# Kernel tuning notes

Hardware: AMD Instinct MI355X
Metric: run time of the kernel (lower is better)

Reference implementation:

```python
import jax, jax.numpy as jnp
import numpy as np

H = 4          # num attention heads
C1 = 64        # channel_num[0]
C2 = 128       # channel_num[1]
KV = C1 + C2   # 192
MLP = C1 * 4   # expand_ratio=4


def _layernorm(x, g, b, eps=1e-6):
    m = jnp.mean(x, axis=-1, keepdims=True)
    v = jnp.mean((x - m) ** 2, axis=-1, keepdims=True)
    return (x - m) * jax.lax.rsqrt(v + eps) * g + b


def setup_inputs() -> dict:
    key = jax.random.key(0)
    ks = jax.random.split(key, 12)
    B, N = 8, 3136
    s_q = 1.0 / np.sqrt(C1)
    s_kv = 1.0 / np.sqrt(KV)
    return {
        "emb1": jax.random.normal(ks[0], (B, N, C1), jnp.float32),
        "emb2": jax.random.normal(ks[1], (B, N, C2), jnp.float32),
        # per-head projection weights (nn.Linear convention: y = x @ W.T)
        "Wq": jax.random.uniform(ks[2], (H, C1, C1), jnp.float32, -s_q, s_q),
        "Wk": jax.random.uniform(ks[3], (H, KV, KV), jnp.float32, -s_kv, s_kv),
        "Wv": jax.random.uniform(ks[4], (H, KV, KV), jnp.float32, -s_kv, s_kv),
        "Wout": jax.random.uniform(ks[5], (C1, C1), jnp.float32, -s_q, s_q),
        "ln1_g": jnp.ones((C1,), jnp.float32),
        "ln1_b": jnp.zeros((C1,), jnp.float32),
        "lnall_g": jnp.ones((KV,), jnp.float32),
        "lnall_b": jnp.zeros((KV,), jnp.float32),
        "ffn_g": jnp.ones((C1,), jnp.float32),
        "ffn_b": jnp.zeros((C1,), jnp.float32),
        "fc1_w": jax.random.uniform(ks[6], (MLP, C1), jnp.float32, -s_q, s_q),
        "fc1_b": jnp.zeros((MLP,), jnp.float32),
        "fc2_w": jax.random.uniform(ks[7], (C1, MLP), jnp.float32, -1.0 / np.sqrt(MLP), 1.0 / np.sqrt(MLP)),
        "fc2_b": jnp.zeros((C1,), jnp.float32),
    }


def reference(emb1, emb2, Wq, Wk, Wv, Wout, ln1_g, ln1_b, lnall_g, lnall_b,
              ffn_g, ffn_b, fc1_w, fc1_b, fc2_w, fc2_b):
    # emb1: [B,N,C1], emb2: [B,N,C2]
    emb_all = jnp.concatenate([emb1, emb2], axis=2)          # [B,N,KV]
    cx1 = _layernorm(emb1, ln1_g, ln1_b)                     # [B,N,C1]
    ea = _layernorm(emb_all, lnall_g, lnall_b)               # [B,N,KV]

    # batched per-head projections (replaces Python loop over ModuleList)
    qT = jnp.einsum('bnc,hdc->bhdn', cx1, Wq)                # [B,H,C1,N]
    k = jnp.einsum('bnk,hdk->bhnd', ea, Wk)                  # [B,H,N,KV]
    vT = jnp.einsum('bnk,hdk->bhdn', ea, Wv)                 # [B,H,KV,N]

    scores = jnp.einsum('bhcn,bhnk->bhck', qT, k) / np.sqrt(KV)  # [B,H,C1,KV]
    # InstanceNorm2d over spatial dims (C1, KV) per (batch, head), affine=False
    m = jnp.mean(scores, axis=(2, 3), keepdims=True)
    v = jnp.mean((scores - m) ** 2, axis=(2, 3), keepdims=True)
    scores = (scores - m) * jax.lax.rsqrt(v + 1e-5)
    probs = jax.nn.softmax(scores, axis=3)                   # softmax over KV

    ctx = jnp.einsum('bhck,bhkn->bhcn', probs, vT)           # [B,H,C1,N]
    ctx = jnp.mean(ctx, axis=1).transpose(0, 2, 1)           # mean over heads -> [B,N,C1]
    o = ctx @ Wout.T                                         # [B,N,C1]

    cx = emb1 + o                                            # residual
    x = _layernorm(cx, ffn_g, ffn_b)
    x = jax.nn.gelu(x @ fc1_w.T + fc1_b, approximate=False)
    x = x @ fc2_w.T + fc2_b
    return x + cx
```

## Files before the change

### kernel.cpp

```cpp
#include <hip/hip_runtime.h>
#include <hip/hip_bf16.h>

typedef __hip_bfloat16 bf;
typedef unsigned short ushort_t;
typedef __attribute__((ext_vector_type(8))) short short8;
typedef __attribute__((ext_vector_type(4))) float f32x4;

#define NB 8
#define SEQ 3136
#define HD 4

__device__ __forceinline__ float lo_bf(unsigned u){ return __uint_as_float(u << 16); }
__device__ __forceinline__ float hi_bf(unsigned u){ return __uint_as_float(u & 0xffff0000u); }
__device__ __forceinline__ float b16f(ushort_t s){ return __uint_as_float(((unsigned)s) << 16); }
__device__ __forceinline__ unsigned short f2bfbits(float f){
  unsigned u = __float_as_uint(f);
  unsigned r = u + 0x7fffu + ((u >> 16) & 1u);
  return (unsigned short)(r >> 16);
}
__device__ __forceinline__ float ldin(const void* p, long i, bool isbf){
  return isbf ? __bfloat162float(((const bf*)p)[i]) : ((const float*)p)[i];
}
__device__ __forceinline__ float4 ld4(const void* p, long i, bool isbf){
  if (isbf){
    uint2 u = *reinterpret_cast<const uint2*>((const unsigned short*)p + i);
    return make_float4(lo_bf(u.x), hi_bf(u.x), lo_bf(u.y), hi_bf(u.y));
  }
  const float* f = (const float*)p + i;
  return make_float4(f[0], f[1], f[2], f[3]);
}
__device__ __forceinline__ short8 ldfrag(const void* p, long i, bool isbf){
  if (isbf) return *reinterpret_cast<const short8*>((const unsigned short*)p + i);
  const float* f = (const float*)p + i;
  short8 r;
  #pragma unroll
  for (int q=0;q<8;++q) r[q] = (short)f2bfbits(f[q]);
  return r;
}
#define DTYPE_FLAG(p) (((const unsigned*)(p))[0] == 0x3F803F80u)

__device__ __forceinline__ float wsum(float v){
  #pragma unroll
  for (int o = 32; o > 0; o >>= 1) v += __shfl_xor(v, o, 64);
  return v;
}
__device__ __forceinline__ float wmax(float v){
  #pragma unroll
  for (int o = 32; o > 0; o >>= 1) v = fmaxf(v, __shfl_xor(v, o, 64));
  return v;
}

__global__ __launch_bounds__(256) void k_g(
    const void* __restrict__ emb1, const void* __restrict__ emb2,
    const void* __restrict__ g1, const void* __restrict__ b1,
    const void* __restrict__ ga, const void* __restrict__ ba,
    ushort_t* __restrict__ part, ushort_t* __restrict__ eag){
  bool isbf = DTYPE_FLAG(g1);
  __shared__ __align__(16) ushort_t z1t[64*72];
  __shared__ __align__(16) ushort_t zat[192*72];
  int tid = threadIdx.x, wave = tid >> 6, lane = tid & 63;
  int quad = lane >> 4, nl = lane & 15;
  int b = blockIdx.y, ch = blockIdx.x;
  long t0 = (long)b*SEQ + ch*64;
  float g1l = ldin(g1,lane,isbf), b1l = ldin(b1,lane,isbf);
  float ga0 = ldin(ga,lane,isbf),     ba0 = ldin(ba,lane,isbf);
  float ga1 = ldin(ga,64+lane,isbf),  ba1 = ldin(ba,64+lane,isbf);
  float ga2 = ldin(ga,128+lane,isbf), ba2 = ldin(ba,128+lane,isbf);
  #pragma unroll 4
  for (int k = 0; k < 16; ++k){
    int tok = wave*16 + k;
    long t = t0 + tok;
    float e1  = ldin(emb1, t*64 + lane, isbf);
    float e2a = ldin(emb2, t*128 + lane, isbf);
    float e2b = ldin(emb2, t*128 + 64 + lane, isbf);
    float s1 = wsum(e1), ss1 = wsum(e1*e1);
    float m1 = s1*(1.f/64.f);
    float r1 = rsqrtf(fmaxf(ss1*(1.f/64.f) - m1*m1, 0.f) + 1e-6f);
    z1t[lane*72 + tok] = f2bfbits((e1 - m1)*r1*g1l + b1l);
    float s23 = wsum(e2a+e2b), ss23 = wsum(e2a*e2a + e2b*e2b);
    float ma = (s1+s23)*(1.f/192.f);
    float ra = rsqrtf(fmaxf((ss1+ss23)*(1.f/192.f) - ma*ma, 0.f) + 1e-6f);
    unsigned short za0 = f2bfbits((e1  - ma)*ra*ga0 + ba0);
    unsigned short za1 = f2bfbits((e2a - ma)*ra*ga1 + ba1);
    unsigned short za2 = f2bfbits((e2b - ma)*ra*ga2 + ba2);
    zat[lane*72 + tok]       = za0;
    zat[(64+lane)*72 + tok]  = za1;
    zat[(128+lane)*72 + tok] = za2;
    eag[t*192 + lane]       = za0;
    eag[t*192 + 64 + lane]  = za1;
    eag[t*192 + 128 + lane] = za2;
  }
  __syncthreads();
  short8 a0 = *reinterpret_cast<const short8*>(&z1t[(wave*16+nl)*72 + quad*8]);
  short8 a1 = *reinterpret_cast<const short8*>(&z1t[(wave*16+nl)*72 + 32 + quad*8]);
  ushort_t* P = part + ((long)b*49 + ch)*12288;
  #pragma unroll
  for (int nt = 0; nt < 12; ++nt){
    f32x4 cd = {0.f,0.f,0.f,0.f};
    short8 b0 = *reinterpret_cast<const short8*>(&zat[(nt*16+nl)*72 + quad*8]);
    cd = __builtin_amdgcn_mfma_f32_16x16x32_bf16(a0, b0, cd, 0, 0, 0);
    short8 b1v = *reinterpret_cast<const short8*>(&zat[(nt*16+nl)*72 + 32 + quad*8]);
    cd = __builtin_amdgcn_mfma_f32_16x16x32_bf16(a1, b1v, cd, 0, 0, 0);
    #pragma unroll
    for (int reg = 0; reg < 4; ++reg)
      P[(wave*16 + quad*4 + reg)*192 + nt*16 + nl] = f2bfbits(cd[reg]);
  }
}

__global__ __launch_bounds__(64) void k_red(
    const ushort_t* __restrict__ part, float* __restrict__ G){
  int idx4 = blockIdx.x*64 + threadIdx.x;
  int b = idx4 / 3072, e4 = idx4 - b*3072;
  const ushort_t* p = part + (long)b*49*12288 + e4*4;
  float s0=0.f, s1=0.f, s2=0.f, s3=0.f;
  #pragma unroll
  for (int ch = 0; ch < 49; ++ch){
    uint2 u = *reinterpret_cast<const uint2*>(p + (long)ch*12288);
    s0 += lo_bf(u.x); s1 += hi_bf(u.x); s2 += lo_bf(u.y); s3 += hi_bf(u.y);
  }
  ((float4*)G)[idx4] = make_float4(s0,s1,s2,s3);
}

__global__ __launch_bounds__(256) void k_s(
    const float* __restrict__ G, const void* __restrict__ Wq, const void* __restrict__ Wk,
    const void* __restrict__ lng, float* __restrict__ S){
  bool isbf = DTYPE_FLAG(lng);
  __shared__ __align__(16) ushort_t sGb[64*200];
  __shared__ __align__(16) ushort_t sT[48*72];
  int ec = blockIdx.x, h = blockIdx.y, b = blockIdx.z;
  int e0 = ec*48;
  int tid = threadIdx.x, wave = tid >> 6, lane = tid & 63;
  int quad = lane >> 4, nl = lane & 15;
  const float4* Gb4 = (const float4*)(G + (long)b*12288);
  for (int i16 = tid; i16 < 3072; i16 += 256){
    float4 v = Gb4[i16];
    int e = i16*4; int c = e/192, j = e - c*192;
    unsigned lo = (unsigned)f2bfbits(v.x) | ((unsigned)f2bfbits(v.y) << 16);
    unsigned hi = (unsigned)f2bfbits(v.z) | ((unsigned)f2bfbits(v.w) << 16);
    *reinterpret_cast<uint2*>(&sGb[c*200 + j]) = make_uint2(lo, hi);
  }
  __syncthreads();
  long wk0 = (long)h*36864;
  short8 aG[6];
  #pragma unroll
  for (int ks = 0; ks < 6; ++ks)
    aG[ks] = *reinterpret_cast<const short8*>(&sGb[(wave*16+nl)*200 + ks*32 + quad*8]);
  #pragma unroll
  for (int nt = 0; nt < 3; ++nt){
    f32x4 cd = {0.f,0.f,0.f,0.f};
    #pragma unroll
    for (int ks = 0; ks < 6; ++ks){
      short8 bw = ldfrag(Wk, wk0 + (long)(e0 + nt*16+nl)*192 + ks*32 + quad*8, isbf);
      cd = __builtin_amdgcn_mfma_f32_16x16x32_bf16(aG[ks], bw, cd, 0, 0, 0);
    }
    #pragma unroll
    for (int reg = 0; reg < 4; ++reg)
      sT[(nt*16+nl)*72 + wave*16 + quad*4 + reg] = f2bfbits(cd[reg]);
  }
  __syncthreads();
  long wq0 = (long)h*4096;
  short8 aQ[2];
  #pragma unroll
  for (int ks = 0; ks < 2; ++ks)
    aQ[ks] = ldfrag(Wq, wq0 + (long)(wave*16+nl)*64 + ks*32 + quad*8, isbf);
  const float scale = 0.07216878364870323f;
  float* Sb = S + ((long)b*HD + h)*12288;
  #pragma unroll
  for (int nt = 0; nt < 3; ++nt){
    f32x4 cd = {0.f,0.f,0.f,0.f};
    #pragma unroll
    for (int ks = 0; ks < 2; ++ks){
      short8 bt = *reinterpret_cast<const short8*>(&sT[(nt*16+nl)*72 + ks*32 + quad*8]);
      cd = __builtin_amdgcn_mfma_f32_16x16x32_bf16(aQ[ks], bt, cd, 0, 0, 0);
    }
    #pragma unroll
    for (int reg = 0; reg < 4; ++reg)
      Sb[(wave*16 + quad*4 + reg)*192 + e0 + nt*16 + nl] = cd[reg]*scale;
  }
}

__global__ __launch_bounds__(256) void k_smpv(
    const float* __restrict__ S, const void* __restrict__ Wv,
    const void* __restrict__ lng, float* __restrict__ Mh){
  bool isbf = DTYPE_FLAG(lng);
  __shared__ __align__(16) float sP[64*196];
  __shared__ __align__(16) unsigned sWv[192*52];
  __shared__ float red[8];
  __shared__ float stat[2];
  int jc = blockIdx.x, h = blockIdx.y, b = blockIdx.z;
  const float* Sb = S + ((long)b*HD + h)*12288;
  int tid = threadIdx.x, wave = tid >> 6, lane = tid & 63;
  long wv0 = (long)h*36864;
  float ps = 0.f, pss = 0.f;
  const float4* Sb4 = (const float4*)Sb;
  for (int i16 = tid; i16 < 3072; i16 += 256){
    float4 v = Sb4[i16];
    int e = i16*4; int c = e/192, j = e - c*192;
    *reinterpret_cast<float4*>(&sP[c*196 + j]) = v;
    ps += v.x + v.y + v.z + v.w;
    pss += v.x*v.x + v.y*v.y + v.z*v.z + v.w*v.w;
  }
  if (isbf){
    const unsigned short* wvp = (const unsigned short*)Wv + wv0 + jc*96;
    for (int idx = tid; idx < 4608; idx += 256){
      int r = idx/24, c2 = idx - r*24;
      uint2 v = *reinterpret_cast<const uint2*>(wvp + (long)r*192 + c2*4);
      *reinterpret_cast<uint2*>(&sWv[r*52 + c2*2]) = v;
    }
  } else {
    for (int idx = tid; idx < 9216; idx += 256){
      int r = idx/48, c = idx - r*48;
      float a0 = ldin(Wv, wv0 + (long)r*192 + jc*96 + c*2,     false);
      float a1 = ldin(Wv, wv0 + (long)r*192 + jc*96 + c*2 + 1, false);
      sWv[r*52 + c] = (unsigned)f2bfbits(a0) | ((unsigned)f2bfbits(a1) << 16);
    }
  }
  ps = wsum(ps); pss = wsum(pss);
  if (lane == 0){ red[wave] = ps; red[4+wave] = pss; }
  __syncthreads();
  if (tid == 0){
    float s  = red[0]+red[1]+red[2]+red[3];
    float s2 = red[4]+red[5]+red[6]+red[7];
    float m = s * (1.f/12288.f);
    stat[0] = m;
    stat[1] = rsqrtf(fmaxf(s2*(1.f/12288.f) - m*m, 0.f) + 1e-5f);
  }
  __syncthreads();
  float m = stat[0], r = stat[1];
  for (int rr = 0; rr < 16; ++rr){
    int row = wave*16 + rr;
    float v0 = (sP[row*196+lane]     - m)*r;
    float v1 = (sP[row*196+64+lane]  - m)*r;
    float v2 = (sP[row*196+128+lane] - m)*r;
    float mx = wmax(fmaxf(v0, fmaxf(v1, v2)));
    float e0 = __expf(v0-mx), e1 = __expf(v1-mx), e2 = __expf(v2-mx);
    float inv = 1.f / wsum(e0+e1+e2);
    sP[row*196+lane]     = e0*inv;
    sP[row*196+64+lane]  = e1*inv;
    sP[row*196+128+lane] = e2*inv;
  }
  __syncthreads();
  int ty = tid >> 4, tx = tid & 15;
  int j0 = jc*96 + tx*6;
  float acc[4][6];
  #pragma unroll
  for (int i=0;i<4;++i) for (int q=0;q<6;++q) acc[i][q]=0.f;
  #pragma unroll 2
  for (int e = 0; e < 192; ++e){
    float p4[4];
    #pragma unroll
    for (int i=0;i<4;++i) p4[i] = sP[(ty*4+i)*196 + e];
    unsigned wa = sWv[e*52 + tx*3];
    unsigned wb = sWv[e*52 + tx*3 + 1];
    unsigned wc = sWv[e*52 + tx*3 + 2];
    float w0 = lo_bf(wa), w1 = hi_bf(wa), w2 = lo_bf(wb),
          w3 = hi_bf(wb), w4 = lo_bf(wc), w5 = hi_bf(wc);
    #pragma unroll
    for (int i=0;i<4;++i){
      acc[i][0] = fmaf(p4[i], w0, acc[i][0]);
      acc[i][1] = fmaf(p4[i], w1, acc[i][1]);
      acc[i][2] = fmaf(p4[i], w2, acc[i][2]);
      acc[i][3] = fmaf(p4[i], w3, acc[i][3]);
      acc[i][4] = fmaf(p4[i], w4, acc[i][4]);
      acc[i][5] = fmaf(p4[i], w5, acc[i][5]);
    }
  }
  float* Mb = Mh + ((long)b*HD + h)*12288;
  #pragma unroll
  for (int i=0;i<4;++i)
    #pragma unroll
    for (int q=0;q<6;++q)
      Mb[(ty*4+i)*192 + j0 + q] = acc[i][q];
}

__global__ __launch_bounds__(256) void k_w2(
    const float* __restrict__ Mh, const void* __restrict__ Wout,
    const void* __restrict__ lng, ushort_t* __restrict__ W2){
  bool isbf = DTYPE_FLAG(lng);
  __shared__ __align__(16) float sM[64*49];
  int jc = blockIdx.x, b = blockIdx.y;
  int tid = threadIdx.x;
  for (int idx = tid; idx < 3072; idx += 256){
    int c = idx/48, j = idx - c*48;
    long base = (long)b*HD*12288 + c*192 + jc*48 + j;
    float s = Mh[base] + Mh[base+12288] + Mh[base+2*12288] + Mh[base+3*12288];
    sM[c*49 + j] = 0.25f*s;
  }
  __syncthreads();
  int ty = tid >> 4, tx = tid & 15;
  float acc[4][3];
  #pragma unroll
  for (int i=0;i<4;++i) for (int q=0;q<3;++q) acc[i][q]=0.f;
  for (int c = 0; c < 64; c += 4){
    float4 w4[4];
    #pragma unroll
    for (int i=0;i<4;++i) w4[i] = ld4(Wout, (long)(ty*4+i)*64 + c, isbf);
    float ww[4][4];
    #pragma unroll
    for (int i=0;i<4;++i){ ww[i][0]=w4[i].x; ww[i][1]=w4[i].y; ww[i][2]=w4[i].z; ww[i][3]=w4[i].w; }
    #pragma unroll
    for (int u = 0; u < 4; ++u){
      float t3[3];
      #pragma unroll
      for (int q=0;q<3;++q) t3[q] = sM[(c+u)*49 + tx*3 + q];
      #pragma unroll
      for (int i=0;i<4;++i)
        #pragma unroll
        for (int q=0;q<3;++q) acc[i][q] = fmaf(ww[i][u], t3[q], acc[i][q]);
    }
  }
  ushort_t* W2b = W2 + (long)b*12288;
  #pragma unroll
  for (int i=0;i<4;++i)
    #pragma unroll
    for (int q=0;q<3;++q)
      W2b[(ty*4+i)*192 + jc*48 + tx*3 + q] = f2bfbits(acc[i][q]);
}

__global__ __launch_bounds__(256) void k_tail(
    const void* __restrict__ emb1, const ushort_t* __restrict__ eag,
    const ushort_t* __restrict__ W2g,
    const void* __restrict__ ffg, const void* __restrict__ ffb,
    const void* __restrict__ f1w, const void* __restrict__ f1b,
    const void* __restrict__ f2w, const void* __restrict__ f2b,
    const void* __restrict__ lng, void* __restrict__ out){
  bool isbf = DTYPE_FLAG(lng);
  __shared__ __align__(16) ushort_t sCX[16*72];
  __shared__ __align__(16) ushort_t sX[16*88];
  __shared__ __align__(16) ushort_t sH[16*280];
  int tid = threadIdx.x, wave = tid >> 6, lane = tid & 63;
  int quad = lane >> 4, nl = lane & 15;
  int b = blockIdx.y;
  long tbase = (long)b*SEQ + blockIdx.x*16;

  short8 aO[6];
  #pragma unroll
  for (int kt = 0; kt < 6; ++kt)
    aO[kt] = *reinterpret_cast<const short8*>(eag + (tbase + nl)*192 + kt*32 + quad*8);
  const ushort_t* W2b = W2g + (long)b*12288;
  {
    f32x4 cd = {0.f,0.f,0.f,0.f};
    #pragma unroll
    for (int kt = 0; kt < 6; ++kt){
      short8 bf8 = *reinterpret_cast<const short8*>(W2b + (wave*16+nl)*192 + kt*32 + quad*8);
      cd = __builtin_amdgcn_mfma_f32_16x16x32_bf16(aO[kt], bf8, cd, 0, 0, 0);
    }
    #pragma unroll
    for (int reg = 0; reg < 4; ++reg){
      int tokl = quad*4 + reg;
      int chn = wave*16 + nl;
      float e1v = ldin(emb1, (tbase + tokl)*64 + chn, isbf);
      sCX[tokl*72 + chn] = f2bfbits(cd[reg] + e1v);
    }
  }
  __syncthreads();

  float gl = ldin(ffg, lane, isbf), bl = ldin(ffb, lane, isbf);
  #pragma unroll
  for (int k = 0; k < 4; ++k){
    int tokl = wave*4 + k;
    float c = b16f(sCX[tokl*72 + lane]);
    float s = wsum(c), ss = wsum(c*c);
    float m = s*(1.f/64.f);
    float r = rsqrtf(fmaxf(ss*(1.f/64.f) - m*m, 0.f) + 1e-6f);
    sX[tokl*88 + lane] = f2bfbits((c - m)*r*gl + bl);
  }
  __syncthreads();

  short8 aX[2];
  #pragma unroll
  for (int kt = 0; kt < 2; ++kt)
    aX[kt] = *reinterpret_cast<const short8*>(&sX[nl*88 + kt*32 + quad*8]);
  #pragma unroll
  for (int nn = 0; nn < 4; ++nn){
    int nt = wave*4 + nn;
    f32x4 cd = {0.f,0.f,0.f,0.f};
    #pragma unroll
    for (int kt = 0; kt < 2; ++kt){
      short8 bf8 = ldfrag(f1w, (long)(nt*16+nl)*64 + kt*32 + quad*8, isbf);
      cd = __builtin_amdgcn_mfma_f32_16x16x32_bf16(aX[kt], bf8, cd, 0, 0, 0);
    }
    float bb = ldin(f1b, nt*16+nl, isbf);
    #pragma unroll
    for (int reg = 0; reg < 4; ++reg){
      float v = cd[reg] + bb;
      float h = 0.5f*v*(1.f + erff(v*0.70710678118654752f));
      sH[(quad*4 + reg)*280 + nt*16 + nl] = f2bfbits(h);
    }
  }
  __syncthreads();

  short8 aH[8];
  #pragma unroll
  for (int kt = 0; kt < 8; ++kt)
    aH[kt] = *reinterpret_cast<const short8*>(&sH[nl*280 + kt*32 + quad*8]);
  {
    f32x4 cd = {0.f,0.f,0.f,0.f};
    #pragma unroll
    for (int kt = 0; kt < 8; ++kt){
      short8 bf8 = ldfrag(f2w, (long)(wave*16+nl)*256 + kt*32 + quad*8, isbf);
      cd = __builtin_amdgcn_mfma_f32_16x16x32_bf16(aH[kt], bf8, cd, 0, 0, 0);
    }
    float bb2 = ldin(f2b, wave*16+nl, isbf);
    #pragma unroll
    for (int reg = 0; reg < 4; ++reg){
      int tokl = quad*4 + reg;
      int chn = wave*16 + nl;
      float y = cd[reg] + bb2 + b16f(sCX[tokl*72 + chn]);
      if (isbf) sCX[tokl*72 + chn] = f2bfbits(y);
      else ((float*)out)[(tbase + tokl)*64 + chn] = y;
    }
  }
  if (isbf){
    __syncthreads();
    int tokl = wave*4 + (lane >> 4), prt = lane & 15;
    uint2 v = *reinterpret_cast<const uint2*>(&sCX[tokl*72 + prt*4]);
    *reinterpret_cast<uint2*>((ushort_t*)out + (tbase + tokl)*64 + prt*4) = v;
  }
}

extern "C" void kernel_launch(void* const* d_in, const int* in_sizes, int n_in,
                              void* d_out, int out_size, void* d_ws, size_t ws_size,
                              hipStream_t stream){
  const void* emb1 = d_in[0];
  const void* emb2 = d_in[1];
  const void* Wq   = d_in[2];
  const void* Wk   = d_in[3];
  const void* Wv   = d_in[4];
  const void* Wout = d_in[5];
  const void* ln1g = d_in[6];
  const void* ln1b = d_in[7];
  const void* lag  = d_in[8];
  const void* lab  = d_in[9];
  const void* ffg  = d_in[10];
  const void* ffb  = d_in[11];
  const void* f1w  = d_in[12];
  const void* f1b  = d_in[13];
  const void* f2w  = d_in[14];
  const void* f2b  = d_in[15];

  char* base = (char*)d_ws;
  ushort_t* part = (ushort_t*)base;
  ushort_t* ea   = (ushort_t*)(base + 9633792);
  float*    G    = (float*)(base + 19267584);
  float*    S    = (float*)(base + 19660800);
  float*    Mh   = (float*)(base + 21233664);
  ushort_t* W2   = (ushort_t*)(base + 22806528);

  k_g   <<<dim3(49,NB),   256, 0, stream>>>(emb1, emb2, ln1g, ln1b, lag, lab, part, ea);
  k_red <<<384,            64, 0, stream>>>(part, G);
  k_s   <<<dim3(4,HD,NB), 256, 0, stream>>>(G, Wq, Wk, ln1g, S);
  k_smpv<<<dim3(2,HD,NB), 256, 0, stream>>>(S, Wv, ln1g, Mh);
  k_w2  <<<dim3(4,NB),    256, 0, stream>>>(Mh, Wout, ln1g, W2);
  k_tail<<<dim3(196,NB),  256, 0, stream>>>(emb1, ea, W2, ffg, ffb,
                                            f1w, f1b, f2w, f2b, ln1g, d_out);
}
```

Measured before the change: 206.2 us.

## Fuse score, softmax and PV into one attention kernel; pre-convert weights to bf16

Merges k_s and k_smpv into a single k_att kernel per (head,batch), so scores stay in shared memory instead of a global round-trip. The PV product moves from scalar FMA to MFMA, with probabilities split into hi/lo bf16 halves to keep precision. Extra blocks in k_g convert the weights once to bf16 (Wv transposed) so later kernels load bf16 fragments directly. The cost is that k_att launches only 32 blocks, so there is less parallelism in that stage.

```diff
diff --git a/kernel.cpp b/kernel.cpp
--- a/kernel.cpp
+++ b/kernel.cpp
@@ -29,13 +29,8 @@
   const float* f = (const float*)p + i;
   return make_float4(f[0], f[1], f[2], f[3]);
 }
-__device__ __forceinline__ short8 ldfrag(const void* p, long i, bool isbf){
-  if (isbf) return *reinterpret_cast<const short8*>((const unsigned short*)p + i);
-  const float* f = (const float*)p + i;
-  short8 r;
-  #pragma unroll
-  for (int q=0;q<8;++q) r[q] = (short)f2bfbits(f[q]);
-  return r;
+__device__ __forceinline__ ushort_t cvt1(const void* p, long i, bool isbf){
+  return isbf ? ((const ushort_t*)p)[i] : f2bfbits(((const float*)p)[i]);
 }
 #define DTYPE_FLAG(p) (((const unsigned*)(p))[0] == 0x3F803F80u)
 
@@ -54,13 +49,33 @@
     const void* __restrict__ emb1, const void* __restrict__ emb2,
     const void* __restrict__ g1, const void* __restrict__ b1,
     const void* __restrict__ ga, const void* __restrict__ ba,
-    ushort_t* __restrict__ part, ushort_t* __restrict__ eag){
+    const void* __restrict__ Wq, const void* __restrict__ Wk, const void* __restrict__ Wv,
+    const void* __restrict__ f1w, const void* __restrict__ f2w,
+    ushort_t* __restrict__ part, ushort_t* __restrict__ eag,
+    ushort_t* __restrict__ Wqb, ushort_t* __restrict__ Wkb, ushort_t* __restrict__ WvTb,
+    ushort_t* __restrict__ f1wb, ushort_t* __restrict__ f2wb){
   bool isbf = DTYPE_FLAG(g1);
+  int tid = threadIdx.x;
+  int b = blockIdx.y, ch = blockIdx.x;
+  if (ch >= 49){
+    if (b != 0) return;
+    int g = (ch - 49)*256 + tid;
+    const int STR = 24*256;
+    for (int i = g; i < 16384; i += STR) Wqb[i] = cvt1(Wq, i, isbf);
+    for (int i = g; i < 147456; i += STR) Wkb[i] = cvt1(Wk, i, isbf);
+    for (int i = g; i < 147456; i += STR){
+      int hh = i / 36864, r = i - hh*36864;
+      int j = r / 192, e = r - j*192;
+      WvTb[i] = cvt1(Wv, (long)hh*36864 + e*192 + j, isbf);
+    }
+    for (int i = g; i < 16384; i += STR) f1wb[i] = cvt1(f1w, i, isbf);
+    for (int i = g; i < 16384; i += STR) f2wb[i] = cvt1(f2w, i, isbf);
+    return;
+  }
   __shared__ __align__(16) ushort_t z1t[64*72];
   __shared__ __align__(16) ushort_t zat[192*72];
-  int tid = threadIdx.x, wave = tid >> 6, lane = tid & 63;
+  int wave = tid >> 6, lane = tid & 63;
   int quad = lane >> 4, nl = lane & 15;
-  int b = blockIdx.y, ch = blockIdx.x;
   long t0 = (long)b*SEQ + ch*64;
   float g1l = ldin(g1,lane,isbf), b1l = ldin(b1,lane,isbf);
   float ga0 = ldin(ga,lane,isbf),     ba0 = ldin(ba,lane,isbf);
@@ -108,7 +123,7 @@
 }
 
 __global__ __launch_bounds__(64) void k_red(
-    const ushort_t* __restrict__ part, float* __restrict__ G){
+    const ushort_t* __restrict__ part, ushort_t* __restrict__ Gb){
   int idx4 = blockIdx.x*64 + threadIdx.x;
   int b = idx4 / 3072, e4 = idx4 - b*3072;
   const ushort_t* p = part + (long)b*49*12288 + e4*4;
@@ -118,39 +133,37 @@
     uint2 u = *reinterpret_cast<const uint2*>(p + (long)ch*12288);
     s0 += lo_bf(u.x); s1 += hi_bf(u.x); s2 += lo_bf(u.y); s3 += hi_bf(u.y);
   }
-  ((float4*)G)[idx4] = make_float4(s0,s1,s2,s3);
-}
-
-__global__ __launch_bounds__(256) void k_s(
-    const float* __restrict__ G, const void* __restrict__ Wq, const void* __restrict__ Wk,
-    const void* __restrict__ lng, float* __restrict__ S){
-  bool isbf = DTYPE_FLAG(lng);
-  __shared__ __align__(16) ushort_t sGb[64*200];
-  __shared__ __align__(16) ushort_t sT[48*72];
-  int ec = blockIdx.x, h = blockIdx.y, b = blockIdx.z;
-  int e0 = ec*48;
+  unsigned lo = (unsigned)f2bfbits(s0) | ((unsigned)f2bfbits(s1) << 16);
+  unsigned hi = (unsigned)f2bfbits(s2) | ((unsigned)f2bfbits(s3) << 16);
+  *reinterpret_cast<uint2*>(Gb + (long)idx4*4) = make_uint2(lo, hi);
+}
+
+__global__ __launch_bounds__(256) void k_att(
+    const ushort_t* __restrict__ Gb, const ushort_t* __restrict__ Wqb,
+    const ushort_t* __restrict__ Wkb, const ushort_t* __restrict__ WvTb,
+    float* __restrict__ Mh){
+  __shared__ __align__(16) ushort_t sT[192*72];
+  __shared__ __align__(16) float    sS[64*196];
+  __shared__ __align__(16) ushort_t sPh[64*200];
+  __shared__ __align__(16) ushort_t sPl[64*200];
+  __shared__ float red[8];
+  __shared__ float stat[2];
+  int h = blockIdx.x, b = blockIdx.y;
   int tid = threadIdx.x, wave = tid >> 6, lane = tid & 63;
   int quad = lane >> 4, nl = lane & 15;
-  const float4* Gb4 = (const float4*)(G + (long)b*12288);
-  for (int i16 = tid; i16 < 3072; i16 += 256){
-    float4 v = Gb4[i16];
-    int e = i16*4; int c = e/192, j = e - c*192;
-    unsigned lo = (unsigned)f2bfbits(v.x) | ((unsigned)f2bfbits(v.y) << 16);
-    unsigned hi = (unsigned)f2bfbits(v.z) | ((unsigned)f2bfbits(v.w) << 16);
-    *reinterpret_cast<uint2*>(&sGb[c*200 + j]) = make_uint2(lo, hi);
-  }
-  __syncthreads();
-  long wk0 = (long)h*36864;
+
+  const ushort_t* Gp = Gb + (long)b*12288;
   short8 aG[6];
   #pragma unroll
   for (int ks = 0; ks < 6; ++ks)
-    aG[ks] = *reinterpret_cast<const short8*>(&sGb[(wave*16+nl)*200 + ks*32 + quad*8]);
-  #pragma unroll
-  for (int nt = 0; nt < 3; ++nt){
+    aG[ks] = *reinterpret_cast<const short8*>(Gp + (wave*16+nl)*192 + ks*32 + quad*8);
+  const ushort_t* Wkp = Wkb + (long)h*36864;
+  #pragma unroll
+  for (int nt = 0; nt < 12; ++nt){
     f32x4 cd = {0.f,0.f,0.f,0.f};
     #pragma unroll
     for (int ks = 0; ks < 6; ++ks){
-      short8 bw = ldfrag(Wk, wk0 + (long)(e0 + nt*16+nl)*192 + ks*32 + quad*8, isbf);
+      short8 bw = *reinterpret_cast<const short8*>(Wkp + (nt*16+nl)*192 + ks*32 + quad*8);
       cd = __builtin_amdgcn_mfma_f32_16x16x32_bf16(aG[ks], bw, cd, 0, 0, 0);
     }
     #pragma unroll
@@ -158,15 +171,16 @@
       sT[(nt*16+nl)*72 + wave*16 + quad*4 + reg] = f2bfbits(cd[reg]);
   }
   __syncthreads();
-  long wq0 = (long)h*4096;
+
+  const ushort_t* Wqp = Wqb + (long)h*4096;
   short8 aQ[2];
   #pragma unroll
   for (int ks = 0; ks < 2; ++ks)
-    aQ[ks] = ldfrag(Wq, wq0 + (long)(wave*16+nl)*64 + ks*32 + quad*8, isbf);
+    aQ[ks] = *reinterpret_cast<const short8*>(Wqp + (wave*16+nl)*64 + ks*32 + quad*8);
   const float scale = 0.07216878364870323f;
-  float* Sb = S + ((long)b*HD + h)*12288;
-  #pragma unroll
-  for (int nt = 0; nt < 3; ++nt){
+  float ps = 0.f, pss = 0.f;
+  #pragma unroll
+  for (int nt = 0; nt < 12; ++nt){
     f32x4 cd = {0.f,0.f,0.f,0.f};
     #pragma unroll
     for (int ks = 0; ks < 2; ++ks){
@@ -174,45 +188,10 @@
       cd = __builtin_amdgcn_mfma_f32_16x16x32_bf16(aQ[ks], bt, cd, 0, 0, 0);
     }
     #pragma unroll
-    for (int reg = 0; reg < 4; ++reg)
-      Sb[(wave*16 + quad*4 + reg)*192 + e0 + nt*16 + nl] = cd[reg]*scale;
-  }
-}
-
-__global__ __launch_bounds__(256) void k_smpv(
-    const float* __restrict__ S, const void* __restrict__ Wv,
-    const void* __restrict__ lng, float* __restrict__ Mh){
-  bool isbf = DTYPE_FLAG(lng);
-  __shared__ __align__(16) float sP[64*196];
-  __shared__ __align__(16) unsigned sWv[192*52];
-  __shared__ float red[8];
-  __shared__ float stat[2];
-  int jc = blockIdx.x, h = blockIdx.y, b = blockIdx.z;
-  const float* Sb = S + ((long)b*HD + h)*12288;
-  int tid = threadIdx.x, wave = tid >> 6, lane = tid & 63;
-  long wv0 = (long)h*36864;
-  float ps = 0.f, pss = 0.f;
-  const float4* Sb4 = (const float4*)Sb;
-  for (int i16 = tid; i16 < 3072; i16 += 256){
-    float4 v = Sb4[i16];
-    int e = i16*4; int c = e/192, j = e - c*192;
-    *reinterpret_cast<float4*>(&sP[c*196 + j]) = v;
-    ps += v.x + v.y + v.z + v.w;
-    pss += v.x*v.x + v.y*v.y + v.z*v.z + v.w*v.w;
-  }
-  if (isbf){
-    const unsigned short* wvp = (const unsigned short*)Wv + wv0 + jc*96;
-    for (int idx = tid; idx < 4608; idx += 256){
-      int r = idx/24, c2 = idx - r*24;
-      uint2 v = *reinterpret_cast<const uint2*>(wvp + (long)r*192 + c2*4);
-      *reinterpret_cast<uint2*>(&sWv[r*52 + c2*2]) = v;
-    }
-  } else {
-    for (int idx = tid; idx < 9216; idx += 256){
-      int r = idx/48, c = idx - r*48;
-      float a0 = ldin(Wv, wv0 + (long)r*192 + jc*96 + c*2,     false);
-      float a1 = ldin(Wv, wv0 + (long)r*192 + jc*96 + c*2 + 1, false);
-      sWv[r*52 + c] = (unsigned)f2bfbits(a0) | ((unsigned)f2bfbits(a1) << 16);
+    for (int reg = 0; reg < 4; ++reg){
+      float v = cd[reg]*scale;
+      sS[(wave*16 + quad*4 + reg)*196 + nt*16 + nl] = v;
+      ps += v; pss += v*v;
     }
   }
   ps = wsum(ps); pss = wsum(pss);
@@ -227,50 +206,44 @@
   }
   __syncthreads();
   float m = stat[0], r = stat[1];
+  #pragma unroll 2
   for (int rr = 0; rr < 16; ++rr){
     int row = wave*16 + rr;
-    float v0 = (sP[row*196+lane]     - m)*r;
-    float v1 = (sP[row*196+64+lane]  - m)*r;
-    float v2 = (sP[row*196+128+lane] - m)*r;
+    float v0 = (sS[row*196+lane]     - m)*r;
+    float v1 = (sS[row*196+64+lane]  - m)*r;
+    float v2 = (sS[row*196+128+lane] - m)*r;
     float mx = wmax(fmaxf(v0, fmaxf(v1, v2)));
     float e0 = __expf(v0-mx), e1 = __expf(v1-mx), e2 = __expf(v2-mx);
     float inv = 1.f / wsum(e0+e1+e2);
-    sP[row*196+lane]     = e0*inv;
-    sP[row*196+64+lane]  = e1*inv;
-    sP[row*196+128+lane] = e2*inv;
-  }
-  __syncthreads();
-  int ty = tid >> 4, tx = tid & 15;
-  int j0 = jc*96 + tx*6;
-  float acc[4][6];
-  #pragma unroll
-  for (int i=0;i<4;++i) for (int q=0;q<6;++q) acc[i][q]=0.f;
-  #pragma unroll 2
-  for (int e = 0; e < 192; ++e){
-    float p4[4];
-    #pragma unroll
-    for (int i=0;i<4;++i) p4[i] = sP[(ty*4+i)*196 + e];
-    unsigned wa = sWv[e*52 + tx*3];
-    unsigned wb = sWv[e*52 + tx*3 + 1];
-    unsigned wc = sWv[e*52 + tx*3 + 2];
-    float w0 = lo_bf(wa), w1 = hi_bf(wa), w2 = lo_bf(wb),
-          w3 = hi_bf(wb), w4 = lo_bf(wc), w5 = hi_bf(wc);
-    #pragma unroll
-    for (int i=0;i<4;++i){
-      acc[i][0] = fmaf(p4[i], w0, acc[i][0]);
-      acc[i][1] = fmaf(p4[i], w1, acc[i][1]);
-      acc[i][2] = fmaf(p4[i], w2, acc[i][2]);
-      acc[i][3] = fmaf(p4[i], w3, acc[i][3]);
-      acc[i][4] = fmaf(p4[i], w4, acc[i][4]);
-      acc[i][5] = fmaf(p4[i], w5, acc[i][5]);
-    }
-  }
+    e0 *= inv; e1 *= inv; e2 *= inv;
+    ushort_t h0 = f2bfbits(e0), h1 = f2bfbits(e1), h2 = f2bfbits(e2);
+    sPh[row*200+lane]     = h0;  sPl[row*200+lane]     = f2bfbits(e0 - b16f(h0));
+    sPh[row*200+64+lane]  = h1;  sPl[row*200+64+lane]  = f2bfbits(e1 - b16f(h1));
+    sPh[row*200+128+lane] = h2;  sPl[row*200+128+lane] = f2bfbits(e2 - b16f(h2));
+  }
+  __syncthreads();
+
+  short8 aPh[6], aPl[6];
+  #pragma unroll
+  for (int ks = 0; ks < 6; ++ks){
+    aPh[ks] = *reinterpret_cast<const short8*>(&sPh[(wave*16+nl)*200 + ks*32 + quad*8]);
+    aPl[ks] = *reinterpret_cast<const short8*>(&sPl[(wave*16+nl)*200 + ks*32 + quad*8]);
+  }
+  const ushort_t* Wvp = WvTb + (long)h*36864;
   float* Mb = Mh + ((long)b*HD + h)*12288;
   #pragma unroll
-  for (int i=0;i<4;++i)
-    #pragma unroll
-    for (int q=0;q<6;++q)
-      Mb[(ty*4+i)*192 + j0 + q] = acc[i][q];
+  for (int nt = 0; nt < 12; ++nt){
+    f32x4 cd = {0.f,0.f,0.f,0.f};
+    #pragma unroll
+    for (int ks = 0; ks < 6; ++ks){
+      short8 bw = *reinterpret_cast<const short8*>(Wvp + (nt*16+nl)*192 + ks*32 + quad*8);
+      cd = __builtin_amdgcn_mfma_f32_16x16x32_bf16(aPl[ks], bw, cd, 0, 0, 0);
+      cd = __builtin_amdgcn_mfma_f32_16x16x32_bf16(aPh[ks], bw, cd, 0, 0, 0);
+    }
+    #pragma unroll
+    for (int reg = 0; reg < 4; ++reg)
+      Mb[(wave*16 + quad*4 + reg)*192 + nt*16 + nl] = cd[reg];
+  }
 }
 
 __global__ __launch_bounds__(256) void k_w2(
@@ -321,8 +294,8 @@
     const void* __restrict__ emb1, const ushort_t* __restrict__ eag,
     const ushort_t* __restrict__ W2g,
     const void* __restrict__ ffg, const void* __restrict__ ffb,
-    const void* __restrict__ f1w, const void* __restrict__ f1b,
-    const void* __restrict__ f2w, const void* __restrict__ f2b,
+    const ushort_t* __restrict__ f1wb, const void* __restrict__ f1b,
+    const ushort_t* __restrict__ f2wb, const void* __restrict__ f2b,
     const void* __restrict__ lng, void* __restrict__ out){
   bool isbf = DTYPE_FLAG(lng);
   __shared__ __align__(16) ushort_t sCX[16*72];
@@ -377,7 +350,7 @@
     f32x4 cd = {0.f,0.f,0.f,0.f};
     #pragma unroll
     for (int kt = 0; kt < 2; ++kt){
-      short8 bf8 = ldfrag(f1w, (long)(nt*16+nl)*64 + kt*32 + quad*8, isbf);
+      short8 bf8 = *reinterpret_cast<const short8*>(f1wb + (long)(nt*16+nl)*64 + kt*32 + quad*8);
       cd = __builtin_amdgcn_mfma_f32_16x16x32_bf16(aX[kt], bf8, cd, 0, 0, 0);
     }
     float bb = ldin(f1b, nt*16+nl, isbf);
@@ -398,7 +371,7 @@
     f32x4 cd = {0.f,0.f,0.f,0.f};
     #pragma unroll
     for (int kt = 0; kt < 8; ++kt){
-      short8 bf8 = ldfrag(f2w, (long)(wave*16+nl)*256 + kt*32 + quad*8, isbf);
+      short8 bf8 = *reinterpret_cast<const short8*>(f2wb + (long)(wave*16+nl)*256 + kt*32 + quad*8);
       cd = __builtin_amdgcn_mfma_f32_16x16x32_bf16(aH[kt], bf8, cd, 0, 0, 0);
     }
     float bb2 = ldin(f2b, wave*16+nl, isbf);
@@ -442,16 +415,21 @@
   char* base = (char*)d_ws;
   ushort_t* part = (ushort_t*)base;
   ushort_t* ea   = (ushort_t*)(base + 9633792);
-  float*    G    = (float*)(base + 19267584);
-  float*    S    = (float*)(base + 19660800);
-  float*    Mh   = (float*)(base + 21233664);
-  ushort_t* W2   = (ushort_t*)(base + 22806528);
-
-  k_g   <<<dim3(49,NB),   256, 0, stream>>>(emb1, emb2, ln1g, ln1b, lag, lab, part, ea);
-  k_red <<<384,            64, 0, stream>>>(part, G);
-  k_s   <<<dim3(4,HD,NB), 256, 0, stream>>>(G, Wq, Wk, ln1g, S);
-  k_smpv<<<dim3(2,HD,NB), 256, 0, stream>>>(S, Wv, ln1g, Mh);
+  ushort_t* Gb   = (ushort_t*)(base + 19267584);
+  float*    Mh   = (float*)(base + 19464192);
+  ushort_t* W2   = (ushort_t*)(base + 21037056);
+  ushort_t* Wqb  = (ushort_t*)(base + 21233664);
+  ushort_t* Wkb  = (ushort_t*)(base + 21266432);
+  ushort_t* WvTb = (ushort_t*)(base + 21561344);
+  ushort_t* f1wb = (ushort_t*)(base + 21856256);
+  ushort_t* f2wb = (ushort_t*)(base + 21889024);
+
+  k_g   <<<dim3(73,NB),   256, 0, stream>>>(emb1, emb2, ln1g, ln1b, lag, lab,
+                                            Wq, Wk, Wv, f1w, f2w,
+                                            part, ea, Wqb, Wkb, WvTb, f1wb, f2wb);
+  k_red <<<384,            64, 0, stream>>>(part, Gb);
+  k_att <<<dim3(HD,NB),   256, 0, stream>>>(Gb, Wqb, Wkb, WvTb, Mh);
   k_w2  <<<dim3(4,NB),    256, 0, stream>>>(Mh, Wout, ln1g, W2);
   k_tail<<<dim3(196,NB),  256, 0, stream>>>(emb1, ea, W2, ffg, ffb,
-                                            f1w, f1b, f2w, f2b, ln1g, d_out);
-}
+                                            f1wb, f1b, f2wb, f2b, ln1g, d_out);
+}
```

Measured after the change: 183.4 us. 11.0% less time.
